# Optimization experiments

Hardware: AMD Instinct MI355X
Metric: run time of the kernel (lower is better)

Reference implementation:

```python
import jax, jax.numpy as jnp
import numpy as np

B, NBC, H, W, HID, OUT = 4, 128, 64, 64, 64, 1
NINT = H * W

def _lin_init(key, fan_in, fan_out):
    kw, kb = jax.random.split(key)
    bound = 1.0 / np.sqrt(fan_in)
    w = jax.random.uniform(kw, (fan_in, fan_out), minval=-bound, maxval=bound, dtype=jnp.float32)
    b = jax.random.uniform(kb, (fan_out,), minval=-bound, maxval=bound, dtype=jnp.float32)
    return w, b

def setup_inputs() -> dict:
    key = jax.random.key(0)
    ks = jax.random.split(key, 7)
    boundary_info = jax.random.normal(ks[0], (B, NBC, 3), dtype=jnp.float32)
    interior_coords = jax.random.uniform(ks[1], (B, NINT, 2), minval=-1.0, maxval=1.0, dtype=jnp.float32)
    W0, b0 = _lin_init(ks[2], 3, HID)        # boundary_encoder layer 0
    W1, b1 = _lin_init(ks[3], HID, HID)      # boundary_encoder layer 1
    G0w, G0b = _lin_init(ks[4], HID + 2, HID)  # green_kernel layer 0
    G1w, G1b = _lin_init(ks[5], HID, HID)      # green_kernel layer 1
    G2w, G2b = _lin_init(ks[6], HID, OUT)      # green_kernel layer 2
    return {"boundary_info": boundary_info, "interior_coords": interior_coords,
            "W0": W0, "b0": b0, "W1": W1, "b1": b1,
            "G0w": G0w, "G0b": G0b, "G1w": G1w, "G1b": G1b,
            "G2w": G2w, "G2b": G2b,
            "interior_h": H, "interior_w": W}

def reference(boundary_info, interior_coords, W0, b0, W1, b1,
              G0w, G0b, G1w, G1b, G2w, G2b, interior_h, interior_w):
    batch, n_bc, _ = boundary_info.shape
    hid = W0.shape[1]
    # boundary encoder: (B, NBC, HID)
    bf = jax.nn.relu(boundary_info @ W0 + b0)
    bf = jax.nn.relu(bf @ W1 + b1)
    # green kernel layer 0: split weight over concat([bf, coords]) so the
    # concatenated (B,NBC,NINT,HID+2) tensor is never materialized.
    a = bf @ G0w[:hid]                      # (B, NBC, HID)
    c = interior_coords @ G0w[hid:]         # (B, NINT, HID)
    h1 = jax.nn.relu(a[:, :, None, :] + c[:, None, :, :] + G0b)  # (B,NBC,NINT,HID)
    h2 = jax.nn.relu(h1 @ G1w + G1b)        # (B, NBC, NINT, HID)
    contribution = h2 @ G2w + G2b           # (B, NBC, NINT, OUT)
    u = contribution.sum(axis=1) / n_bc     # (B, NINT, OUT)
    return u.reshape(batch, 1, interior_h, interior_w)
```

## Files before the change

kernel.cpp:

```cpp
#include <hip/hip_runtime.h>
#include <hip/hip_bf16.h>

#define BB   4
#define NBC  128
#define NINT 4096
#define HID  64

using short8  = __attribute__((ext_vector_type(8)))  short;
using float16 = __attribute__((ext_vector_type(16))) float;

static __device__ __forceinline__ short f2bf(float f) {
    __hip_bfloat16 h = __float2bfloat16(f);
    return __builtin_bit_cast(short, h);
}
static __device__ __forceinline__ unsigned fbits(float f) {
    return __builtin_bit_cast(unsigned, f);
}
static __device__ __forceinline__ unsigned pack_bf_trunc(float lo, float hi) {
    return __builtin_amdgcn_perm(fbits(hi), fbits(lo), 0x07060302u);
}

__global__ void __launch_bounds__(256) bge_prep(
    const float* __restrict__ binfo,
    const float* __restrict__ W0,
    const float* __restrict__ b0,
    const float* __restrict__ W1,
    const float* __restrict__ b1,
    const float* __restrict__ G0w,
    const float* __restrict__ G0b,
    float* __restrict__ aprime)
{
    __shared__ float sW1[HID * HID];
    __shared__ float sG0[HID * HID];
    __shared__ float shv [4][HID];
    __shared__ float shv2[4][HID];

    const int tid = threadIdx.x;
    const int wv  = tid >> 6;
    const int t   = tid & 63;
    const int row = blockIdx.x * 4 + wv;

    for (int idx = tid; idx < HID * HID / 4; idx += 256) {
        ((float4*)sW1)[idx] = ((const float4*)W1)[idx];
        ((float4*)sG0)[idx] = ((const float4*)G0w)[idx];
    }

    const float x0 = binfo[row*3+0];
    const float x1 = binfo[row*3+1];
    const float x2 = binfo[row*3+2];
    float h = fmaxf(x0*W0[t] + x1*W0[64+t] + x2*W0[128+t] + b0[t], 0.0f);
    shv[wv][t] = h;
    __syncthreads();

    float acc = b1[t];
    #pragma unroll 8
    for (int k = 0; k < HID; ++k) acc += shv[wv][k] * sW1[k*64 + t];
    shv2[wv][t] = fmaxf(acc, 0.0f);
    __syncthreads();

    float a = G0b[t];
    #pragma unroll 8
    for (int k = 0; k < HID; ++k) a += shv2[wv][k] * sG0[k*64 + t];
    aprime[row*HID + t] = a;
}

__global__ void __launch_bounds__(256) bge_main(
    const float* __restrict__ icoord,
    const float* __restrict__ G0w,
    const float* __restrict__ G1w,
    const float* __restrict__ G1b,
    const float* __restrict__ G2w,
    const float* __restrict__ G2b,
    const float* __restrict__ aprime,
    float* __restrict__ out)
{
    __shared__ float sred[4][64];

    const int b    = blockIdx.y;
    const int i0   = blockIdx.x * 32;
    const int tid  = threadIdx.x;
    const int wv   = tid >> 6;
    const int lane = tid & 63;
    const int hf   = lane >> 5;
    const int ln   = lane & 31;

    const float2 cc = ((const float2*)icoord)[(size_t)b*NINT + i0 + ln];
    float cre[4][8];
    #pragma unroll
    for (int st = 0; st < 4; ++st)
        #pragma unroll
        for (int jj = 0; jj < 8; ++jj) {
            const int k = st*16 + hf*8 + jj;
            cre[st][jj] = cc.x*G0w[64*64 + k] + cc.y*G0w[65*64 + k];
        }

    short8 afr[2][4];
    #pragma unroll
    for (int t = 0; t < 2; ++t)
        #pragma unroll
        for (int st = 0; st < 4; ++st)
            #pragma unroll
            for (int jj = 0; jj < 8; ++jj) {
                const int k = st*16 + hf*8 + jj;
                afr[t][st][jj] = f2bf(G1w[k*64 + t*32 + ln]);
            }

    float g2c[2][16];
    #pragma unroll
    for (int t = 0; t < 2; ++t)
        #pragma unroll
        for (int r = 0; r < 16; ++r)
            g2c[t][r] = G2w[(r&3) + 8*(r>>2) + 4*hf + 32*t];

    float16 accb0, accb1;
    {
        short8 afb0 = (short8)0, afb1 = (short8)0, bone = (short8)0;
        if (hf == 0) {
            afb0[0] = f2bf(G1b[ln]);
            afb1[0] = f2bf(G1b[32 + ln]);
            bone[0] = (short)0x3F80;
        }
        const float16 zc = (float16)0.0f;
        accb0 = __builtin_amdgcn_mfma_f32_32x32x16_bf16(afb0, bone, zc, 0, 0, 0);
        accb1 = __builtin_amdgcn_mfma_f32_32x32x16_bf16(afb1, bone, zc, 0, 0, 0);
    }

    float s0 = 0.0f, s1 = 0.0f, s2 = 0.0f, s3 = 0.0f;

    const float* arow = aprime + ((size_t)b*NBC + wv*32)*HID;
    #pragma unroll 2
    for (int it = 0; it < 32; ++it, arow += HID) {
        short8 bf[4];
        #pragma unroll
        for (int st = 0; st < 4; ++st) {
            const float4 v0 = *(const float4*)(arow + st*16 + hf*8);
            const float4 v1 = *(const float4*)(arow + st*16 + hf*8 + 4);
            const float e0 = fmaxf(v0.x + cre[st][0], 0.0f);
            const float e1 = fmaxf(v0.y + cre[st][1], 0.0f);
            const float e2 = fmaxf(v0.z + cre[st][2], 0.0f);
            const float e3 = fmaxf(v0.w + cre[st][3], 0.0f);
            const float e4 = fmaxf(v1.x + cre[st][4], 0.0f);
            const float e5 = fmaxf(v1.y + cre[st][5], 0.0f);
            const float e6 = fmaxf(v1.z + cre[st][6], 0.0f);
            const float e7 = fmaxf(v1.w + cre[st][7], 0.0f);
            int di0 = (int)pack_bf_trunc(e0, e1);
            int di1 = (int)pack_bf_trunc(e2, e3);
            int di2 = (int)pack_bf_trunc(e4, e5);
            int di3 = (int)pack_bf_trunc(e6, e7);
            bf[st][0] = (short)(di0 & 0xFFFF); bf[st][1] = (short)(((unsigned)di0) >> 16);
            bf[st][2] = (short)(di1 & 0xFFFF); bf[st][3] = (short)(((unsigned)di1) >> 16);
            bf[st][4] = (short)(di2 & 0xFFFF); bf[st][5] = (short)(((unsigned)di2) >> 16);
            bf[st][6] = (short)(di3 & 0xFFFF); bf[st][7] = (short)(((unsigned)di3) >> 16);
        }
        float16 acc0 = __builtin_amdgcn_mfma_f32_32x32x16_bf16(afr[0][0], bf[0], accb0, 0, 0, 0);
        float16 acc1 = __builtin_amdgcn_mfma_f32_32x32x16_bf16(afr[1][0], bf[0], accb1, 0, 0, 0);
        #pragma unroll
        for (int st = 1; st < 4; ++st) {
            acc0 = __builtin_amdgcn_mfma_f32_32x32x16_bf16(afr[0][st], bf[st], acc0, 0, 0, 0);
            acc1 = __builtin_amdgcn_mfma_f32_32x32x16_bf16(afr[1][st], bf[st], acc1, 0, 0, 0);
        }
        #pragma unroll
        for (int r = 0; r < 16; r += 4) {
            s0 += fmaxf(acc0[r+0], 0.0f)*g2c[0][r+0] + fmaxf(acc1[r+0], 0.0f)*g2c[1][r+0];
            s1 += fmaxf(acc0[r+1], 0.0f)*g2c[0][r+1] + fmaxf(acc1[r+1], 0.0f)*g2c[1][r+1];
            s2 += fmaxf(acc0[r+2], 0.0f)*g2c[0][r+2] + fmaxf(acc1[r+2], 0.0f)*g2c[1][r+2];
            s3 += fmaxf(acc0[r+3], 0.0f)*g2c[0][r+3] + fmaxf(acc1[r+3], 0.0f)*g2c[1][r+3];
        }
    }

    sred[wv][lane] = (s0 + s1) + (s2 + s3);
    __syncthreads();

    if (tid < 32) {
        float tot = 0.0f;
        #pragma unroll
        for (int w = 0; w < 4; ++w) tot += sred[w][tid] + sred[w][tid + 32];
        out[(size_t)b*NINT + i0 + tid] = tot * (1.0f/128.0f) + G2b[0];
    }
}

extern "C" void kernel_launch(void* const* d_in, const int* in_sizes, int n_in,
                              void* d_out, int out_size, void* d_ws, size_t ws_size,
                              hipStream_t stream) {
    const float* binfo  = (const float*)d_in[0];
    const float* icoord = (const float*)d_in[1];
    const float* W0     = (const float*)d_in[2];
    const float* b0     = (const float*)d_in[3];
    const float* W1     = (const float*)d_in[4];
    const float* b1     = (const float*)d_in[5];
    const float* G0w    = (const float*)d_in[6];
    const float* G0b    = (const float*)d_in[7];
    const float* G1w    = (const float*)d_in[8];
    const float* G1b    = (const float*)d_in[9];
    const float* G2w    = (const float*)d_in[10];
    const float* G2b    = (const float*)d_in[11];

    float* aprime = (float*)d_ws;

    hipLaunchKernelGGL(bge_prep, dim3(BB*NBC/4), dim3(256), 0, stream,
                       binfo, W0, b0, W1, b1, G0w, G0b, aprime);
    hipLaunchKernelGGL(bge_main, dim3(NINT/32, BB), dim3(256), 0, stream,
                       icoord, G0w, G1w, G1b, G2w, G2b, aprime,
                       (float*)d_out);
}
```

Before: 123.2 us.

## Switch to 16x16x32 MFMA, split boundary rows across blocks with atomics

Replaces the 32x32x16 MFMA layout with 16x16x32 MFMAs. The h1 tile now feeds the A operand and G1w sits in B fragments. The G1b bias moves out of the MFMA and into the ReLU threshold (max against -b1), with a constant correction term added at the end. This removes the bias MFMAs and the accumulator seeding. The NBC loop is split over two blocks in grid z, which combine their results through atomicAdd into an output that the prep kernel now zeroes, doubling parallelism. The per-wave reduction uses lane shuffles, and the arithmetic uses packed float2 operations, at the cost of float atomics and a nondeterministic summation order.

```diff
diff --git a/kernel.cpp b/kernel.cpp
--- a/kernel.cpp
+++ b/kernel.cpp
@@ -7,7 +7,9 @@
 #define HID  64
 
 using short8  = __attribute__((ext_vector_type(8)))  short;
-using float16 = __attribute__((ext_vector_type(16))) float;
+using float4v = __attribute__((ext_vector_type(4)))  float;
+using f2      = __attribute__((ext_vector_type(2)))  float;
+using int4v   = __attribute__((ext_vector_type(4)))  int;
 
 static __device__ __forceinline__ short f2bf(float f) {
     __hip_bfloat16 h = __float2bfloat16(f);
@@ -28,7 +30,8 @@
     const float* __restrict__ b1,
     const float* __restrict__ G0w,
     const float* __restrict__ G0b,
-    float* __restrict__ aprime)
+    float* __restrict__ aprime,
+    float* __restrict__ out)
 {
     __shared__ float sW1[HID * HID];
     __shared__ float sG0[HID * HID];
@@ -39,6 +42,9 @@
     const int wv  = tid >> 6;
     const int t   = tid & 63;
     const int row = blockIdx.x * 4 + wv;
+
+    const int g = blockIdx.x * 256 + tid;
+    if (g < BB * NINT) out[g] = 0.0f;
 
     for (int idx = tid; idx < HID * HID / 4; idx += 256) {
         ((float4*)sW1)[idx] = ((const float4*)W1)[idx];
@@ -74,108 +80,121 @@
     const float* __restrict__ aprime,
     float* __restrict__ out)
 {
-    __shared__ float sred[4][64];
+    __shared__ float sred[4][32];
 
     const int b    = blockIdx.y;
     const int i0   = blockIdx.x * 32;
+    const int zh   = blockIdx.z;
     const int tid  = threadIdx.x;
     const int wv   = tid >> 6;
     const int lane = tid & 63;
-    const int hf   = lane >> 5;
-    const int ln   = lane & 31;
-
-    const float2 cc = ((const float2*)icoord)[(size_t)b*NINT + i0 + ln];
-    float cre[4][8];
-    #pragma unroll
-    for (int st = 0; st < 4; ++st)
+    const int ln   = lane & 15;
+    const int q    = lane >> 4;
+
+    const float2 cc0 = ((const float2*)icoord)[(size_t)b*NINT + i0 + ln];
+    const float2 cc1 = ((const float2*)icoord)[(size_t)b*NINT + i0 + 16 + ln];
+
+    f2 cre[2][2][4];
+    #pragma unroll
+    for (int kh = 0; kh < 2; ++kh)
         #pragma unroll
         for (int jj = 0; jj < 8; ++jj) {
-            const int k = st*16 + hf*8 + jj;
-            cre[st][jj] = cc.x*G0w[64*64 + k] + cc.y*G0w[65*64 + k];
+            const int k = kh*32 + q*8 + jj;
+            const float gx = G0w[64*64 + k], gy = G0w[65*64 + k];
+            cre[0][kh][jj>>1][jj&1] = cc0.x*gx + cc0.y*gy;
+            cre[1][kh][jj>>1][jj&1] = cc1.x*gx + cc1.y*gy;
         }
 
-    short8 afr[2][4];
-    #pragma unroll
-    for (int t = 0; t < 2; ++t)
-        #pragma unroll
-        for (int st = 0; st < 4; ++st)
-            #pragma unroll
-            for (int jj = 0; jj < 8; ++jj) {
-                const int k = st*16 + hf*8 + jj;
-                afr[t][st][jj] = f2bf(G1w[k*64 + t*32 + ln]);
+    short8 bfrag[2][4];
+    #pragma unroll
+    for (int kh = 0; kh < 2; ++kh)
+        #pragma unroll
+        for (int nt = 0; nt < 4; ++nt)
+            #pragma unroll
+            for (int jj = 0; jj < 8; ++jj)
+                bfrag[kh][nt][jj] = f2bf(G1w[(kh*32 + q*8 + jj)*64 + nt*16 + ln]);
+
+    float nb1[4], g2v[4];
+    float corr = 0.0f;
+    #pragma unroll
+    for (int nt = 0; nt < 4; ++nt) {
+        const float bv = G1b[nt*16 + ln];
+        const float gv = G2w[nt*16 + ln];
+        nb1[nt] = -bv;  g2v[nt] = gv;  corr += bv * gv;
+    }
+
+    f2 s[2][2];
+    s[0][0] = (f2)0.0f; s[0][1] = (f2)0.0f; s[1][0] = (f2)0.0f; s[1][1] = (f2)0.0f;
+    const float4v zc4 = (float4v)0.0f;
+
+    const float* arow = aprime + ((size_t)b*NBC + zh*64 + wv*16)*HID;
+    #pragma unroll 1
+    for (int it = 0; it < 16; ++it, arow += HID) {
+        short8 af[2][2];
+        #pragma unroll
+        for (int kh = 0; kh < 2; ++kh) {
+            const float4 v0 = *(const float4*)(arow + kh*32 + q*8);
+            const float4 v1 = *(const float4*)(arow + kh*32 + q*8 + 4);
+            f2 w[4];
+            w[0][0]=v0.x; w[0][1]=v0.y; w[1][0]=v0.z; w[1][1]=v0.w;
+            w[2][0]=v1.x; w[2][1]=v1.y; w[3][0]=v1.z; w[3][1]=v1.w;
+            #pragma unroll
+            for (int ih = 0; ih < 2; ++ih) {
+                const f2 e0 = w[0] + cre[ih][kh][0];
+                const f2 e1 = w[1] + cre[ih][kh][1];
+                const f2 e2 = w[2] + cre[ih][kh][2];
+                const f2 e3 = w[3] + cre[ih][kh][3];
+                int4v di;
+                di[0] = (int)pack_bf_trunc(fmaxf(e0[0],0.f), fmaxf(e0[1],0.f));
+                di[1] = (int)pack_bf_trunc(fmaxf(e1[0],0.f), fmaxf(e1[1],0.f));
+                di[2] = (int)pack_bf_trunc(fmaxf(e2[0],0.f), fmaxf(e2[1],0.f));
+                di[3] = (int)pack_bf_trunc(fmaxf(e3[0],0.f), fmaxf(e3[1],0.f));
+                af[ih][kh] = __builtin_bit_cast(short8, di);
             }
-
-    float g2c[2][16];
-    #pragma unroll
-    for (int t = 0; t < 2; ++t)
-        #pragma unroll
-        for (int r = 0; r < 16; ++r)
-            g2c[t][r] = G2w[(r&3) + 8*(r>>2) + 4*hf + 32*t];
-
-    float16 accb0, accb1;
-    {
-        short8 afb0 = (short8)0, afb1 = (short8)0, bone = (short8)0;
-        if (hf == 0) {
-            afb0[0] = f2bf(G1b[ln]);
-            afb1[0] = f2bf(G1b[32 + ln]);
-            bone[0] = (short)0x3F80;
         }
-        const float16 zc = (float16)0.0f;
-        accb0 = __builtin_amdgcn_mfma_f32_32x32x16_bf16(afb0, bone, zc, 0, 0, 0);
-        accb1 = __builtin_amdgcn_mfma_f32_32x32x16_bf16(afb1, bone, zc, 0, 0, 0);
-    }
-
-    float s0 = 0.0f, s1 = 0.0f, s2 = 0.0f, s3 = 0.0f;
-
-    const float* arow = aprime + ((size_t)b*NBC + wv*32)*HID;
-    #pragma unroll 2
-    for (int it = 0; it < 32; ++it, arow += HID) {
-        short8 bf[4];
-        #pragma unroll
-        for (int st = 0; st < 4; ++st) {
-            const float4 v0 = *(const float4*)(arow + st*16 + hf*8);
-            const float4 v1 = *(const float4*)(arow + st*16 + hf*8 + 4);
-            const float e0 = fmaxf(v0.x + cre[st][0], 0.0f);
-            const float e1 = fmaxf(v0.y + cre[st][1], 0.0f);
-            const float e2 = fmaxf(v0.z + cre[st][2], 0.0f);
-            const float e3 = fmaxf(v0.w + cre[st][3], 0.0f);
-            const float e4 = fmaxf(v1.x + cre[st][4], 0.0f);
-            const float e5 = fmaxf(v1.y + cre[st][5], 0.0f);
-            const float e6 = fmaxf(v1.z + cre[st][6], 0.0f);
-            const float e7 = fmaxf(v1.w + cre[st][7], 0.0f);
-            int di0 = (int)pack_bf_trunc(e0, e1);
-            int di1 = (int)pack_bf_trunc(e2, e3);
-            int di2 = (int)pack_bf_trunc(e4, e5);
-            int di3 = (int)pack_bf_trunc(e6, e7);
-            bf[st][0] = (short)(di0 & 0xFFFF); bf[st][1] = (short)(((unsigned)di0) >> 16);
-            bf[st][2] = (short)(di1 & 0xFFFF); bf[st][3] = (short)(((unsigned)di1) >> 16);
-            bf[st][4] = (short)(di2 & 0xFFFF); bf[st][5] = (short)(((unsigned)di2) >> 16);
-            bf[st][6] = (short)(di3 & 0xFFFF); bf[st][7] = (short)(((unsigned)di3) >> 16);
-        }
-        float16 acc0 = __builtin_amdgcn_mfma_f32_32x32x16_bf16(afr[0][0], bf[0], accb0, 0, 0, 0);
-        float16 acc1 = __builtin_amdgcn_mfma_f32_32x32x16_bf16(afr[1][0], bf[0], accb1, 0, 0, 0);
-        #pragma unroll
-        for (int st = 1; st < 4; ++st) {
-            acc0 = __builtin_amdgcn_mfma_f32_32x32x16_bf16(afr[0][st], bf[st], acc0, 0, 0, 0);
-            acc1 = __builtin_amdgcn_mfma_f32_32x32x16_bf16(afr[1][st], bf[st], acc1, 0, 0, 0);
-        }
-        #pragma unroll
-        for (int r = 0; r < 16; r += 4) {
-            s0 += fmaxf(acc0[r+0], 0.0f)*g2c[0][r+0] + fmaxf(acc1[r+0], 0.0f)*g2c[1][r+0];
-            s1 += fmaxf(acc0[r+1], 0.0f)*g2c[0][r+1] + fmaxf(acc1[r+1], 0.0f)*g2c[1][r+1];
-            s2 += fmaxf(acc0[r+2], 0.0f)*g2c[0][r+2] + fmaxf(acc1[r+2], 0.0f)*g2c[1][r+2];
-            s3 += fmaxf(acc0[r+3], 0.0f)*g2c[0][r+3] + fmaxf(acc1[r+3], 0.0f)*g2c[1][r+3];
-        }
-    }
-
-    sred[wv][lane] = (s0 + s1) + (s2 + s3);
+        #pragma unroll
+        for (int ih = 0; ih < 2; ++ih)
+            #pragma unroll
+            for (int nt = 0; nt < 4; ++nt) {
+                float4v acc = __builtin_amdgcn_mfma_f32_16x16x32_bf16(
+                                  af[ih][0], bfrag[0][nt], zc4, 0, 0, 0);
+                acc = __builtin_amdgcn_mfma_f32_16x16x32_bf16(
+                                  af[ih][1], bfrag[1][nt], acc, 0, 0, 0);
+                f2 m0, m1;
+                m0[0] = fmaxf(acc[0], nb1[nt]); m0[1] = fmaxf(acc[1], nb1[nt]);
+                m1[0] = fmaxf(acc[2], nb1[nt]); m1[1] = fmaxf(acc[3], nb1[nt]);
+                s[ih][0] += m0 * g2v[nt];
+                s[ih][1] += m1 * g2v[nt];
+            }
+    }
+
+    const f2 cadd = (f2)(16.0f * corr);
+    s[0][0] += cadd; s[0][1] += cadd; s[1][0] += cadd; s[1][1] += cadd;
+
+    float v8[8] = { s[0][0][0], s[0][0][1], s[0][1][0], s[0][1][1],
+                    s[1][0][0], s[1][0][1], s[1][1][0], s[1][1][1] };
+    #pragma unroll
+    for (int t = 0; t < 8; ++t) {
+        float v = v8[t];
+        v += __shfl_xor(v, 1);
+        v += __shfl_xor(v, 2);
+        v += __shfl_xor(v, 4);
+        v += __shfl_xor(v, 8);
+        v8[t] = v;
+    }
+    if (ln == 0) {
+        #pragma unroll
+        for (int ih = 0; ih < 2; ++ih)
+            #pragma unroll
+            for (int r = 0; r < 4; ++r)
+                sred[wv][ih*16 + q*4 + r] = v8[ih*4 + r];
+    }
     __syncthreads();
 
     if (tid < 32) {
-        float tot = 0.0f;
-        #pragma unroll
-        for (int w = 0; w < 4; ++w) tot += sred[w][tid] + sred[w][tid + 32];
-        out[(size_t)b*NINT + i0 + tid] = tot * (1.0f/128.0f) + G2b[0];
+        const float tot = sred[0][tid] + sred[1][tid] + sred[2][tid] + sred[3][tid];
+        atomicAdd(out + (size_t)b*NINT + i0 + tid,
+                  tot * (1.0f/128.0f) + 0.5f * G2b[0]);
     }
 }
 
@@ -198,8 +217,8 @@
     float* aprime = (float*)d_ws;
 
     hipLaunchKernelGGL(bge_prep, dim3(BB*NBC/4), dim3(256), 0, stream,
-                       binfo, W0, b0, W1, b1, G0w, G0b, aprime);
-    hipLaunchKernelGGL(bge_main, dim3(NINT/32, BB), dim3(256), 0, stream,
+                       binfo, W0, b0, W1, b1, G0w, G0b, aprime, (float*)d_out);
+    hipLaunchKernelGGL(bge_main, dim3(NINT/32, BB, 2), dim3(256), 0, stream,
                        icoord, G0w, G1w, G1b, G2w, G2b, aprime,
                        (float*)d_out);
 }
```

New measurement: 121.0 us. Within noise of the previous version (-1.8%).
